# Performance work log

Hardware: AMD Instinct MI355X
Metric: run time of the kernel (lower is better)

## Reference

```python
import jax, jax.numpy as jnp
import numpy as np

N = 4_194_304  # total points
C = 2          # classes: 0=ground, 1=plant
B = 8          # number of point clouds in the batch
SIGMA_L = 0.1
SIGMA_R = 0.4
CLAMP_FACTOR = 2.0
MIN_VAL = 0.1
FOCAL_GAMMA = 2.0
FOCAL_ALPHA = 1.0
LOSS_WEIGHT = 1.0


def setup_inputs() -> dict:
    key = jax.random.key(0)
    k1, k2, k3 = jax.random.split(key, 3)
    pred = jax.random.normal(k1, (N, C), dtype=jnp.float32)
    coord = jax.random.normal(k2, (N, 3), dtype=jnp.float32)
    segment = jax.random.randint(k3, (N,), 0, C, dtype=jnp.int32)
    # pointcept-style cumulative offsets: equal-sized clouds, offset[-1] == N
    offset = (jnp.arange(1, B + 1, dtype=jnp.int32) * (N // B))
    return {"pred": pred, "coord": coord, "segment": segment, "offset": offset}


def _gauss_weights(z, segment, batch):
    # per-cloud z_ground_max (fallback: z.min) and z_plant_min (fallback: z.max)
    neg_inf = jnp.array(-jnp.inf, z.dtype)
    pos_inf = jnp.array(jnp.inf, z.dtype)
    gmax = jax.ops.segment_max(jnp.where(segment == 0, z, neg_inf), batch, num_segments=B)
    pmin = jax.ops.segment_min(jnp.where(segment == 1, z, pos_inf), batch, num_segments=B)
    has_g = jax.ops.segment_sum((segment == 0).astype(z.dtype), batch, num_segments=B) > 0
    has_p = jax.ops.segment_sum((segment == 1).astype(z.dtype), batch, num_segments=B) > 0
    zmin = jax.ops.segment_min(z, batch, num_segments=B)
    zmax = jax.ops.segment_max(z, batch, num_segments=B)
    g = jnp.where(has_g, gmax, zmin)
    p = jnp.where(has_p, pmin, zmax)
    mu_b = g + (p - g) * 0.5  # (B,)
    mu = mu_b[batch]          # (N,)
    d = z - mu
    w_left = jnp.exp(-(d * d) / (2.0 * SIGMA_L * SIGMA_L))
    w_right = jnp.exp(-(d * d) / (2.0 * SIGMA_R * SIGMA_R))
    w_right = jnp.where(d > CLAMP_FACTOR * SIGMA_R, jnp.array(MIN_VAL, z.dtype), w_right)
    return jnp.where(z <= mu, w_left, w_right)


def reference(pred, coord, segment, offset):
    n = pred.shape[0]
    # offset2batch: per-point batch id from cumulative offsets
    batch = jnp.searchsorted(offset, jnp.arange(n, dtype=offset.dtype), side='right')
    # cross entropy (reduction='none')
    logp = jax.nn.log_softmax(pred, axis=1)              # (N, C)
    logp_t = jnp.take_along_axis(logp, segment[:, None], axis=1)[:, 0]  # (N,)
    seg_loss = (-logp_t) * LOSS_WEIGHT
    # focal reweighting (computed under no_grad in the original)
    p_t = jax.lax.stop_gradient(jnp.exp(logp_t))
    focal_weight = FOCAL_ALPHA * (1.0 - p_t) ** FOCAL_GAMMA
    seg_loss = seg_loss * focal_weight
    # asymmetric gaussian z-weighting, segment-conditioned per cloud
    weights = _gauss_weights(coord[:, 2], segment, batch)
    return jnp.mean(seg_loss * weights)
```

## Files before the change

kernel.cpp:

```cpp
#include <hip/hip_runtime.h>
#include <math.h>

#define THREADS 1024
#define NBLOCKS 256
#define UNROLL  8

__device__ __forceinline__ unsigned enc_f(float f) {
    unsigned b = __float_as_uint(f);
    return (b & 0x80000000u) ? ~b : (b | 0x80000000u);
}
__device__ __forceinline__ float dec_f(unsigned u) {
    unsigned b = (u & 0x80000000u) ? (u ^ 0x80000000u) : ~u;
    return __uint_as_float(b);
}
#define ENC_NEG_INF 0x007FFFFFu
#define ENC_POS_INF 0xFF800000u
__device__ __forceinline__ unsigned ident_w(int w) {
    return (w < 8 || w >= 24) ? ENC_NEG_INF : ENC_POS_INF;
}

#define SLOT(base, blk) ((base) + 64 + (blk) * 32)

#define CNT_B(ii, bdst) do { bdst = 0; \
    _Pragma("unroll") for (int j_ = 0; j_ < 8; ++j_) bdst += ((ii) >= roff[j_]); } while (0)

#define FLUSH_LDS(bb, g_, p_, mn_, mx_) do { \
    atomicMax(&s_stats[      (bb)], enc_f(g_));  \
    atomicMin(&s_stats[ 8  + (bb)], enc_f(p_));  \
    atomicMin(&s_stats[16  + (bb)], enc_f(mn_)); \
    atomicMax(&s_stats[24  + (bb)], enc_f(mx_)); } while (0)

__global__ __launch_bounds__(THREADS) void k_stats(
        const float* __restrict__ coord, const int* __restrict__ segment,
        const int* __restrict__ offset, unsigned* __restrict__ ws, int n, int nb) {
    __shared__ unsigned s_stats[32];
    const int tid = threadIdx.x;
    if (tid < 32) s_stats[tid] = ident_w(tid);
    if (blockIdx.x == 0 && tid == THREADS - 1) {
        *(double*)(ws + 32) = 0.0;
        ws[34] = 0u;
    }
    int roff[8];
    #pragma unroll
    for (int j = 0; j < 8; ++j) roff[j] = (j < nb) ? offset[j] : 0x7FFFFFFF;
    __syncthreads();

    const int chunk = (n + (int)gridDim.x - 1) / (int)gridDim.x;
    const int start = blockIdx.x * chunk;
    const int end   = min(n, start + chunk);

    float lg = -INFINITY, lp = INFINITY, lmn = INFINITY, lmx = -INFINITY;

    if (start < end) {
        int ba = 0, bb = 0;
        #pragma unroll
        for (int j = 0; j < 8; ++j) { ba += (start >= roff[j]); bb += ((end - 1) >= roff[j]); }
        if (ba == bb) {
            int i = start + tid;
            for (; i + (UNROLL - 1) * THREADS < end; i += UNROLL * THREADS) {
                float z[UNROLL]; int s[UNROLL];
                #pragma unroll
                for (int k = 0; k < UNROLL; ++k) z[k] = coord[3 * (i + k * THREADS) + 2];
                #pragma unroll
                for (int k = 0; k < UNROLL; ++k) s[k] = segment[i + k * THREADS];
                #pragma unroll
                for (int k = 0; k < UNROLL; ++k) {
                    lmn = fminf(lmn, z[k]);
                    lmx = fmaxf(lmx, z[k]);
                    lg  = fmaxf(lg, (s[k] == 0) ? z[k] : -INFINITY);
                    lp  = fminf(lp, (s[k] != 0) ? z[k] : INFINITY);
                }
            }
            for (; i < end; i += THREADS) {
                float z = coord[3 * i + 2]; int s = segment[i];
                lmn = fminf(lmn, z); lmx = fmaxf(lmx, z);
                lg  = fmaxf(lg, (s == 0) ? z : -INFINITY);
                lp  = fminf(lp, (s != 0) ? z : INFINITY);
            }
            #pragma unroll
            for (int m = 32; m; m >>= 1) {
                lg  = fmaxf(lg,  __shfl_xor(lg,  m, 64));
                lp  = fminf(lp,  __shfl_xor(lp,  m, 64));
                lmn = fminf(lmn, __shfl_xor(lmn, m, 64));
                lmx = fmaxf(lmx, __shfl_xor(lmx, m, 64));
            }
            if ((tid & 63) == 0) FLUSH_LDS(ba, lg, lp, lmn, lmx);
        } else {
            int curb = -1;
            for (int i = start + tid; i < end; i += THREADS) {
                float z = coord[3 * i + 2]; int s = segment[i], b;
                CNT_B(i, b);
                if (b != curb) {
                    if (curb >= 0) FLUSH_LDS(curb, lg, lp, lmn, lmx);
                    lg = -INFINITY; lp = INFINITY; lmn = INFINITY; lmx = -INFINITY;
                    curb = b;
                }
                lmn = fminf(lmn, z); lmx = fmaxf(lmx, z);
                if (s == 0) lg = fmaxf(lg, z); else lp = fminf(lp, z);
            }
            if (curb >= 0) FLUSH_LDS(curb, lg, lp, lmn, lmx);
        }
    }
    __syncthreads();
    if (tid < 32) SLOT(ws, blockIdx.x)[tid] = s_stats[tid];
}

__device__ __forceinline__ float point_loss(float p0, float p1, int s, float z, float mu) {
    float m   = fmaxf(p0, p1);
    float lse = m + logf(expf(p0 - m) + expf(p1 - m));
    float lpt = ((s == 0) ? p0 : p1) - lse;
    float pt  = expf(lpt);
    float om  = 1.0f - pt;
    float loss = -lpt * om * om;
    float d  = z - mu;
    float cf = (z <= mu) ? 50.0f : 3.125f;
    float w  = expf(-d * d * cf);
    if (z > mu && d > 0.8f) w = 0.1f;
    return loss * w;
}

__global__ __launch_bounds__(THREADS) void k_loss(
        const float* __restrict__ pred, const float* __restrict__ coord,
        const int* __restrict__ segment, const int* __restrict__ offset,
        unsigned* __restrict__ ws, float* __restrict__ out, int n, int nb) {
    __shared__ unsigned s_comb[32];
    __shared__ float    s_mu[8];
    __shared__ float    s_part[THREADS / 64];
    const int tid = threadIdx.x;
    int roff[8];
    #pragma unroll
    for (int j = 0; j < 8; ++j) roff[j] = (j < nb) ? offset[j] : 0x7FFFFFFF;

    if (tid < 32) s_comb[tid] = ident_w(tid);
    __syncthreads();
    {
        const int w = tid & 31, g = tid >> 5;
        unsigned v = ident_w(w);
        #pragma unroll
        for (int j = 0; j < NBLOCKS / 32; ++j) {
            unsigned u = SLOT((const unsigned*)ws, g * (NBLOCKS / 32) + j)[w];
            v = (w < 8 || w >= 24) ? max(v, u) : min(v, u);
        }
        if (w < 8 || w >= 24) atomicMax(&s_comb[w], v);
        else                  atomicMin(&s_comb[w], v);
    }
    __syncthreads();
    if (tid < 8) {
        unsigned ug = s_comb[tid], up = s_comb[8 + tid];
        float g = dec_f(ug), p = dec_f(up);
        if (ug == ENC_NEG_INF) g = dec_f(s_comb[16 + tid]);
        if (up == ENC_POS_INF) p = dec_f(s_comb[24 + tid]);
        s_mu[tid] = g + (p - g) * 0.5f;
    }
    __syncthreads();

    const int chunk = (n + (int)gridDim.x - 1) / (int)gridDim.x;
    const int start = blockIdx.x * chunk;
    const int end   = min(n, start + chunk);
    const float2* pred2 = (const float2*)pred;

    float lsum = 0.0f;
    if (start < end) {
        int ba = 0, bb = 0;
        #pragma unroll
        for (int j = 0; j < 8; ++j) { ba += (start >= roff[j]); bb += ((end - 1) >= roff[j]); }
        if (ba == bb) {
            const float mu = s_mu[ba];
            int i = start + tid;
            for (; i + (UNROLL - 1) * THREADS < end; i += UNROLL * THREADS) {
                float z[UNROLL]; int s[UNROLL]; float2 pp[UNROLL];
                #pragma unroll
                for (int k = 0; k < UNROLL; ++k) pp[k] = pred2[i + k * THREADS];
                #pragma unroll
                for (int k = 0; k < UNROLL; ++k) z[k] = coord[3 * (i + k * THREADS) + 2];
                #pragma unroll
                for (int k = 0; k < UNROLL; ++k) s[k] = segment[i + k * THREADS];
                #pragma unroll
                for (int k = 0; k < UNROLL; ++k)
                    lsum += point_loss(pp[k].x, pp[k].y, s[k], z[k], mu);
            }
            for (; i < end; i += THREADS) {
                float2 pp = pred2[i];
                lsum += point_loss(pp.x, pp.y, segment[i], coord[3 * i + 2], mu);
            }
        } else {
            for (int i = start + tid; i < end; i += THREADS) {
                int b; CNT_B(i, b);
                float2 pp = pred2[i];
                lsum += point_loss(pp.x, pp.y, segment[i], coord[3 * i + 2], s_mu[b]);
            }
        }
    }

    #pragma unroll
    for (int off = 32; off > 0; off >>= 1) lsum += __shfl_down(lsum, off, 64);
    if ((tid & 63) == 0) s_part[tid >> 6] = lsum;
    __syncthreads();
    if (tid == 0) {
        float t = 0.0f;
        #pragma unroll
        for (int wv = 0; wv < THREADS / 64; ++wv) t += s_part[wv];
        double* acc = (double*)(ws + 32);
        atomicAdd(acc, (double)t);
        __threadfence();
        unsigned c = atomicAdd(&ws[34], 1u);
        if (c == (unsigned)gridDim.x - 1u) {
            double v = atomicAdd(acc, 0.0);
            out[0] = (float)(v / (double)n);
        }
    }
}

extern "C" void kernel_launch(void* const* d_in, const int* in_sizes, int n_in,
                              void* d_out, int out_size, void* d_ws, size_t ws_size,
                              hipStream_t stream) {
    const float* pred    = (const float*)d_in[0];
    const float* coord   = (const float*)d_in[1];
    const int*   segment = (const int*)d_in[2];
    const int*   offset  = (const int*)d_in[3];
    const int n  = in_sizes[2];
    const int nb = in_sizes[3];

    unsigned* ws = (unsigned*)d_ws;

    hipLaunchKernelGGL(k_stats, dim3(NBLOCKS), dim3(THREADS), 0, stream,
                       coord, segment, offset, ws, n, nb);
    hipLaunchKernelGGL(k_loss,  dim3(NBLOCKS), dim3(THREADS), 0, stream,
                       pred, coord, segment, offset, ws, (float*)d_out, n, nb);
}
```

Before: 133.6 us.

## Stage coord through LDS with coalesced float4 loads in both kernels

```diff
diff --git a/kernel.cpp b/kernel.cpp
--- a/kernel.cpp
+++ b/kernel.cpp
@@ -3,7 +3,8 @@
 
 #define THREADS 1024
 #define NBLOCKS 256
-#define UNROLL  8
+#define SUBPTS  4096
+#define CHUNK   (4 * SUBPTS)
 
 __device__ __forceinline__ unsigned enc_f(float f) {
     unsigned b = __float_as_uint(f);
@@ -33,6 +34,7 @@
 __global__ __launch_bounds__(THREADS) void k_stats(
         const float* __restrict__ coord, const int* __restrict__ segment,
         const int* __restrict__ offset, unsigned* __restrict__ ws, int n, int nb) {
+    __shared__ float    s_c[3 * SUBPTS];
     __shared__ unsigned s_stats[32];
     const int tid = threadIdx.x;
     if (tid < 32) s_stats[tid] = ident_w(tid);
@@ -51,55 +53,59 @@
 
     float lg = -INFINITY, lp = INFINITY, lmn = INFINITY, lmx = -INFINITY;
 
+    int ba = 0, bz = 0;
     if (start < end) {
-        int ba = 0, bb = 0;
-        #pragma unroll
-        for (int j = 0; j < 8; ++j) { ba += (start >= roff[j]); bb += ((end - 1) >= roff[j]); }
-        if (ba == bb) {
-            int i = start + tid;
-            for (; i + (UNROLL - 1) * THREADS < end; i += UNROLL * THREADS) {
-                float z[UNROLL]; int s[UNROLL];
-                #pragma unroll
-                for (int k = 0; k < UNROLL; ++k) z[k] = coord[3 * (i + k * THREADS) + 2];
-                #pragma unroll
-                for (int k = 0; k < UNROLL; ++k) s[k] = segment[i + k * THREADS];
-                #pragma unroll
-                for (int k = 0; k < UNROLL; ++k) {
-                    lmn = fminf(lmn, z[k]);
-                    lmx = fmaxf(lmx, z[k]);
-                    lg  = fmaxf(lg, (s[k] == 0) ? z[k] : -INFINITY);
-                    lp  = fminf(lp, (s[k] != 0) ? z[k] : INFINITY);
-                }
+        #pragma unroll
+        for (int j = 0; j < 8; ++j) { ba += (start >= roff[j]); bz += ((end - 1) >= roff[j]); }
+    }
+    const bool fast = (start < end) && (ba == bz) && (end - start == CHUNK) && (chunk == CHUNK);
+
+    if (fast) {
+        float4* s4 = (float4*)s_c;
+        #pragma unroll
+        for (int st = 0; st < 4; ++st) {
+            const int   base = start + st * SUBPTS;
+            const float4* cg4 = (const float4*)coord + ((size_t)base * 3 >> 2);
+            float4 c0 = cg4[tid], c1 = cg4[tid + 1024], c2 = cg4[tid + 2048];
+            int4   sg = ((const int4*)segment)[(base >> 2) + tid];
+            s4[tid] = c0; s4[tid + 1024] = c1; s4[tid + 2048] = c2;
+            __syncthreads();
+            float z0 = s_c[12*tid + 2], z1 = s_c[12*tid + 5];
+            float z2 = s_c[12*tid + 8], z3 = s_c[12*tid + 11];
+            lmn = fminf(fminf(fminf(lmn, z0), z1), fminf(z2, z3));
+            lmx = fmaxf(fmaxf(fmaxf(lmx, z0), z1), fmaxf(z2, z3));
+            lg  = fmaxf(lg, (sg.x == 0) ? z0 : -INFINITY);
+            lg  = fmaxf(lg, (sg.y == 0) ? z1 : -INFINITY);
+            lg  = fmaxf(lg, (sg.z == 0) ? z2 : -INFINITY);
+            lg  = fmaxf(lg, (sg.w == 0) ? z3 : -INFINITY);
+            lp  = fminf(lp, (sg.x != 0) ? z0 : INFINITY);
+            lp  = fminf(lp, (sg.y != 0) ? z1 : INFINITY);
+            lp  = fminf(lp, (sg.z != 0) ? z2 : INFINITY);
+            lp  = fminf(lp, (sg.w != 0) ? z3 : INFINITY);
+            __syncthreads();
+        }
+        #pragma unroll
+        for (int m = 32; m; m >>= 1) {
+            lg  = fmaxf(lg,  __shfl_xor(lg,  m, 64));
+            lp  = fminf(lp,  __shfl_xor(lp,  m, 64));
+            lmn = fminf(lmn, __shfl_xor(lmn, m, 64));
+            lmx = fmaxf(lmx, __shfl_xor(lmx, m, 64));
+        }
+        if ((tid & 63) == 0) FLUSH_LDS(ba, lg, lp, lmn, lmx);
+    } else if (start < end) {
+        int curb = -1;
+        for (int i = start + tid; i < end; i += THREADS) {
+            float z = coord[3 * i + 2]; int s = segment[i], b;
+            CNT_B(i, b);
+            if (b != curb) {
+                if (curb >= 0) FLUSH_LDS(curb, lg, lp, lmn, lmx);
+                lg = -INFINITY; lp = INFINITY; lmn = INFINITY; lmx = -INFINITY;
+                curb = b;
             }
-            for (; i < end; i += THREADS) {
-                float z = coord[3 * i + 2]; int s = segment[i];
-                lmn = fminf(lmn, z); lmx = fmaxf(lmx, z);
-                lg  = fmaxf(lg, (s == 0) ? z : -INFINITY);
-                lp  = fminf(lp, (s != 0) ? z : INFINITY);
-            }
-            #pragma unroll
-            for (int m = 32; m; m >>= 1) {
-                lg  = fmaxf(lg,  __shfl_xor(lg,  m, 64));
-                lp  = fminf(lp,  __shfl_xor(lp,  m, 64));
-                lmn = fminf(lmn, __shfl_xor(lmn, m, 64));
-                lmx = fmaxf(lmx, __shfl_xor(lmx, m, 64));
-            }
-            if ((tid & 63) == 0) FLUSH_LDS(ba, lg, lp, lmn, lmx);
-        } else {
-            int curb = -1;
-            for (int i = start + tid; i < end; i += THREADS) {
-                float z = coord[3 * i + 2]; int s = segment[i], b;
-                CNT_B(i, b);
-                if (b != curb) {
-                    if (curb >= 0) FLUSH_LDS(curb, lg, lp, lmn, lmx);
-                    lg = -INFINITY; lp = INFINITY; lmn = INFINITY; lmx = -INFINITY;
-                    curb = b;
-                }
-                lmn = fminf(lmn, z); lmx = fmaxf(lmx, z);
-                if (s == 0) lg = fmaxf(lg, z); else lp = fminf(lp, z);
-            }
-            if (curb >= 0) FLUSH_LDS(curb, lg, lp, lmn, lmx);
-        }
+            lmn = fminf(lmn, z); lmx = fmaxf(lmx, z);
+            if (s == 0) lg = fmaxf(lg, z); else lp = fminf(lp, z);
+        }
+        if (curb >= 0) FLUSH_LDS(curb, lg, lp, lmn, lmx);
     }
     __syncthreads();
     if (tid < 32) SLOT(ws, blockIdx.x)[tid] = s_stats[tid];
@@ -123,6 +129,7 @@
         const float* __restrict__ pred, const float* __restrict__ coord,
         const int* __restrict__ segment, const int* __restrict__ offset,
         unsigned* __restrict__ ws, float* __restrict__ out, int n, int nb) {
+    __shared__ float    s_c[3 * SUBPTS];
     __shared__ unsigned s_comb[32];
     __shared__ float    s_mu[8];
     __shared__ float    s_part[THREADS / 64];
@@ -159,36 +166,42 @@
     const int end   = min(n, start + chunk);
     const float2* pred2 = (const float2*)pred;
 
+    int ba = 0, bz = 0;
+    if (start < end) {
+        #pragma unroll
+        for (int j = 0; j < 8; ++j) { ba += (start >= roff[j]); bz += ((end - 1) >= roff[j]); }
+    }
+    const bool fast = (start < end) && (ba == bz) && (end - start == CHUNK) && (chunk == CHUNK);
+
     float lsum = 0.0f;
-    if (start < end) {
-        int ba = 0, bb = 0;
-        #pragma unroll
-        for (int j = 0; j < 8; ++j) { ba += (start >= roff[j]); bb += ((end - 1) >= roff[j]); }
-        if (ba == bb) {
-            const float mu = s_mu[ba];
-            int i = start + tid;
-            for (; i + (UNROLL - 1) * THREADS < end; i += UNROLL * THREADS) {
-                float z[UNROLL]; int s[UNROLL]; float2 pp[UNROLL];
-                #pragma unroll
-                for (int k = 0; k < UNROLL; ++k) pp[k] = pred2[i + k * THREADS];
-                #pragma unroll
-                for (int k = 0; k < UNROLL; ++k) z[k] = coord[3 * (i + k * THREADS) + 2];
-                #pragma unroll
-                for (int k = 0; k < UNROLL; ++k) s[k] = segment[i + k * THREADS];
-                #pragma unroll
-                for (int k = 0; k < UNROLL; ++k)
-                    lsum += point_loss(pp[k].x, pp[k].y, s[k], z[k], mu);
+    if (fast) {
+        const float mu = s_mu[ba];
+        float4* s4 = (float4*)s_c;
+        #pragma unroll
+        for (int st = 0; st < 4; ++st) {
+            const int   base = start + st * SUBPTS;
+            const float4* cg4 = (const float4*)coord + ((size_t)base * 3 >> 2);
+            float4 c0 = cg4[tid], c1 = cg4[tid + 1024], c2 = cg4[tid + 2048];
+            float2 pp[4]; int sg[4];
+            #pragma unroll
+            for (int k = 0; k < 4; ++k) pp[k] = pred2[base + tid + k * 1024];
+            #pragma unroll
+            for (int k = 0; k < 4; ++k) sg[k] = segment[base + tid + k * 1024];
+            s4[tid] = c0; s4[tid + 1024] = c1; s4[tid + 2048] = c2;
+            __syncthreads();
+            #pragma unroll
+            for (int k = 0; k < 4; ++k) {
+                const int m = tid + k * 1024;
+                const float z = s_c[3 * m + 2];
+                lsum += point_loss(pp[k].x, pp[k].y, sg[k], z, mu);
             }
-            for (; i < end; i += THREADS) {
-                float2 pp = pred2[i];
-                lsum += point_loss(pp.x, pp.y, segment[i], coord[3 * i + 2], mu);
-            }
-        } else {
-            for (int i = start + tid; i < end; i += THREADS) {
-                int b; CNT_B(i, b);
-                float2 pp = pred2[i];
-                lsum += point_loss(pp.x, pp.y, segment[i], coord[3 * i + 2], s_mu[b]);
-            }
+            __syncthreads();
+        }
+    } else if (start < end) {
+        for (int i = start + tid; i < end; i += THREADS) {
+            int b; CNT_B(i, b);
+            float2 pp = pred2[i];
+            lsum += point_loss(pp.x, pp.y, segment[i], coord[3 * i + 2], s_mu[b]);
         }
     }
 
```

Result: slower. 136.7 us (+2.3%).
